# Kernel tuning notes

Measured on AMD Instinct MI355X. Metric: run time of the kernel, lower is better.

Reference implementation:

```python
import jax, jax.numpy as jnp
import numpy as np

N_C = 50000
N_N = 50000
E = 500000
D = 128


def _graph_conv(x_src, src, dst, n_src, n_dst, W, b):
    # DGL GraphConv, norm='both': symmetric degree normalization, then linear.
    ones = jnp.ones(src.shape, x_src.dtype)
    deg_out = jax.ops.segment_sum(ones, src, num_segments=n_src)
    deg_in = jax.ops.segment_sum(ones, dst, num_segments=n_dst)
    norm_src = jnp.maximum(deg_out, 1.0) ** -0.5  # [n_src]
    norm_dst = jnp.maximum(deg_in, 1.0) ** -0.5   # [n_dst]
    m = (x_src * norm_src[:, None])[src]          # [E, D] gather
    agg = jax.ops.segment_sum(m, dst, num_segments=n_dst)  # [n_dst, D]
    return (agg * norm_dst[:, None]) @ W + b


def _sage_conv(x_src, x_dst, src, dst, n_dst, W_self, W_neigh, b):
    # DGL SAGEConv, aggregator='mean': fc_self(h_dst) + fc_neigh(mean_neigh) + bias.
    ones = jnp.ones(src.shape, x_src.dtype)
    deg_in = jnp.maximum(jax.ops.segment_sum(ones, dst, num_segments=n_dst), 1.0)
    h_neigh = jax.ops.segment_sum(x_src[src], dst, num_segments=n_dst) / deg_in[:, None]
    return x_dst @ W_self + h_neigh @ W_neigh + b


def setup_inputs() -> dict:
    key = jax.random.key(0)
    ks = jax.random.split(key, 20)
    s = 1.0 / np.sqrt(D)
    inp = {
        'feat_C': jax.random.normal(ks[0], (N_C, D), jnp.float32),
        'feat_N': jax.random.normal(ks[1], (N_N, D), jnp.float32),
        'W1_cc': jax.random.normal(ks[2], (D, D), jnp.float32) * s,
        'b1_cc': jnp.zeros((D,), jnp.float32),
        'W1_cn': jax.random.normal(ks[3], (D, D), jnp.float32) * s,
        'b1_cn': jnp.zeros((D,), jnp.float32),
        'W1_self': jax.random.normal(ks[4], (D, D), jnp.float32) * s,
        'W1_neigh': jax.random.normal(ks[5], (D, D), jnp.float32) * s,
        'b1_nn': jnp.zeros((D,), jnp.float32),
        'W2_cc': jax.random.normal(ks[6], (D, D), jnp.float32) * s,
        'b2_cc': jnp.zeros((D,), jnp.float32),
        'W2_cn': jax.random.normal(ks[7], (D, D), jnp.float32) * s,
        'b2_cn': jnp.zeros((D,), jnp.float32),
        'W2_self': jax.random.normal(ks[8], (D, D), jnp.float32) * s,
        'W2_neigh': jax.random.normal(ks[9], (D, D), jnp.float32) * s,
        'b2_nn': jnp.zeros((D,), jnp.float32),
        'cc_src': jax.random.randint(ks[10], (E,), 0, N_C),
        'cc_dst': jax.random.randint(ks[11], (E,), 0, N_C),
        'cn_src': jax.random.randint(ks[12], (E,), 0, N_C),
        'cn_dst': jax.random.randint(ks[13], (E,), 0, N_N),
        'nn_src': jax.random.randint(ks[14], (E,), 0, N_N),
        'nn_dst': jax.random.randint(ks[15], (E,), 0, N_N),
    }
    return inp


def reference(feat_C, feat_N, W1_cc, b1_cc, W1_cn, b1_cn, W1_self, W1_neigh, b1_nn,
              W2_cc, b2_cc, W2_cn, b2_cn, W2_self, W2_neigh, b2_nn,
              cc_src, cc_dst, cn_src, cn_dst, nn_src, nn_dst):
    # layer 1 (HeteroGraphConv, aggregate='sum') + relu
    hC = _graph_conv(feat_C, cc_src, cc_dst, N_C, N_C, W1_cc, b1_cc)
    hN = (_graph_conv(feat_C, cn_src, cn_dst, N_C, N_N, W1_cn, b1_cn)
          + _sage_conv(feat_N, feat_N, nn_src, nn_dst, N_N, W1_self, W1_neigh, b1_nn))
    hC = jax.nn.relu(hC)
    hN = jax.nn.relu(hN)
    # layer 2
    oC = _graph_conv(hC, cc_src, cc_dst, N_C, N_C, W2_cc, b2_cc)
    oN = (_graph_conv(hC, cn_src, cn_dst, N_C, N_N, W2_cn, b2_cn)
          + _sage_conv(hN, hN, nn_src, nn_dst, N_N, W2_self, W2_neigh, b2_nn))
    return oC, oN
```

## Files before the change

kernel.cpp:

```cpp
#include <hip/hip_runtime.h>

#define NCN 50000
#define NE  500000
#define DF  128

#define BSHIFT 9
#define NBUCK 98
#define BK 128
#define CAP 7168
#define CHUNK 4096

typedef __attribute__((ext_vector_type(8))) short mfrag;
typedef __attribute__((ext_vector_type(4))) float facc4;

__device__ inline ushort f2bf(float x) {
    unsigned u = __float_as_uint(x);
    unsigned r = (u + 0x7FFFu + ((u >> 16) & 1u)) >> 16;
    return (ushort)r;
}
__device__ inline float bf2f(ushort h) { return __uint_as_float(((unsigned)h) << 16); }

__device__ inline void store_split4m(ushort* __restrict__ T, int row, int lane4,
                                     float4 v, int mode) {
    ushort h0 = f2bf(v.x); ushort l0 = f2bf(v.x - bf2f(h0));
    ushort h1 = f2bf(v.y); ushort l1 = f2bf(v.y - bf2f(h1));
    ushort h2 = f2bf(v.z); ushort l2 = f2bf(v.z - bf2f(h2));
    ushort h3 = f2bf(v.w); ushort l3 = f2bf(v.w - bf2f(h3));
    uint2 hp = make_uint2((uint)h0 | ((uint)h1 << 16), (uint)h2 | ((uint)h3 << 16));
    uint2 lp = make_uint2((uint)l0 | ((uint)l1 << 16), (uint)l2 | ((uint)l3 << 16));
    size_t hiOff, loOff;
    if (mode == 0) { hiOff = (size_t)row * DF; loOff = (size_t)NCN * DF + (size_t)row * DF; }
    else           { hiOff = (size_t)row * 256; loOff = hiOff + 128; }
    *(uint2*)(T + hiOff + lane4 * 4) = hp;
    *(uint2*)(T + loOff + lane4 * 4) = lp;
}

__global__ __launch_bounds__(256) void hist2_k(
    const int* __restrict__ cc_src, const int* __restrict__ cn_src,
    int* __restrict__ cnt2)
{
    int i = blockIdx.x * 256 + threadIdx.x;
    if (i >= NE) return;
    atomicAdd(&cnt2[cc_src[i]], 1);
    atomicAdd(&cnt2[NCN + cn_src[i]], 1);
}

__global__ __launch_bounds__(256) void srcnorm_k(
    const int* __restrict__ cnt2, float* __restrict__ snorm2, int n2)
{
    int i = blockIdx.x * 256 + threadIdx.x;
    if (i >= n2) return;
    int c = cnt2[i]; if (c < 1) c = 1;
    snorm2[i] = rsqrtf((float)c);
}

__global__ __launch_bounds__(256) void binA_k(
    const int* __restrict__ cc_src, const int* __restrict__ cc_dst,
    const int* __restrict__ cn_src, const int* __restrict__ cn_dst,
    const int* __restrict__ nn_src, const int* __restrict__ nn_dst,
    uint2* __restrict__ R, int* __restrict__ bc)
{
    const int s = blockIdx.y;
    const int* key; const int* pay;
    switch (s) {
      case 0: key = cc_dst; pay = cc_src; break;
      case 1: key = cn_dst; pay = cn_src; break;
      default: key = nn_dst; pay = nn_src; break;
    }
    __shared__ uint2 rec[CHUNK];
    __shared__ int lhist[BK], lofs[BK], lcur[BK], gbase[BK];
    __shared__ int ls[256];
    const int tid = threadIdx.x;
    const int base = blockIdx.x * CHUNK;

    int k[16], p[16];
    #pragma unroll
    for (int j = 0; j < 16; ++j) {
        int e = base + j * 256 + tid;
        bool valid = (e < NE);
        k[j] = valid ? key[e] : -1;
        p[j] = valid ? pay[e] : 0;
    }
    if (tid < BK) lhist[tid] = 0;
    __syncthreads();
    #pragma unroll
    for (int j = 0; j < 16; ++j)
        if (k[j] >= 0) atomicAdd(&lhist[k[j] >> BSHIFT], 1);
    __syncthreads();
    int v = (tid < BK) ? lhist[tid] : 0;
    ls[tid] = v;
    __syncthreads();
    #pragma unroll
    for (int off = 1; off < 128; off <<= 1) {
        int t = (tid >= off) ? ls[tid - off] : 0;
        __syncthreads();
        ls[tid] += t;
        __syncthreads();
    }
    if (tid < BK) { int e = ls[tid] - v; lofs[tid] = e; lcur[tid] = e; }
    __syncthreads();
    #pragma unroll
    for (int j = 0; j < 16; ++j) {
        if (k[j] >= 0) {
            int b = k[j] >> BSHIFT;
            int pos = atomicAdd(&lcur[b], 1);
            rec[pos] = make_uint2((unsigned)k[j], (unsigned)p[j]);
        }
    }
    __syncthreads();
    if (tid < BK) {
        int c = lcur[tid] - lofs[tid];
        gbase[tid] = (c > 0) ? atomicAdd(&bc[s * BK + tid], c) : 0;
    }
    __syncthreads();
    int total = ls[127];
    for (int i = tid; i < total; i += 256) {
        uint2 r = rec[i];
        int b = (int)(r.x >> BSHIFT);
        int gi = gbase[b] + (i - lofs[b]);
        R[((size_t)s * NBUCK + b) * CAP + gi] = r;
    }
}

__global__ __launch_bounds__(256) void binB_k(
    const uint2* __restrict__ R, const int* __restrict__ bc,
    int* __restrict__ rp3, int* __restrict__ col3)
{
    const int b = blockIdx.x;
    const int s = blockIdx.y;
    const int tid = threadIdx.x;
    __shared__ int cnt[512];
    __shared__ int lofs[512];
    __shared__ int ls[256];
    __shared__ int sbase;

    const int nrec = bc[s * BK + b];
    const uint2* rec = R + ((size_t)s * NBUCK + b) * CAP;

    for (int i = tid; i < 512; i += 256) cnt[i] = 0;
    __syncthreads();
    for (int i = tid; i < nrec; i += 256)
        atomicAdd(&cnt[rec[i].x & 511], 1);
    __syncthreads();

    {
        int v = (tid < b) ? bc[s * BK + tid] : 0;
        ls[tid] = v;
        __syncthreads();
        for (int off = 128; off > 0; off >>= 1) {
            if (tid < off) ls[tid] += ls[tid + off];
            __syncthreads();
        }
        if (tid == 0) sbase = ls[0];
        __syncthreads();
    }
    const int colBase = sbase;

    int v0 = cnt[2 * tid], v1 = cnt[2 * tid + 1];
    int pairSum = v0 + v1;
    ls[tid] = pairSum;
    __syncthreads();
    #pragma unroll
    for (int off = 1; off < 256; off <<= 1) {
        int t = (tid >= off) ? ls[tid - off] : 0;
        __syncthreads();
        ls[tid] += t;
        __syncthreads();
    }
    int excl = ls[tid] - pairSum;
    lofs[2 * tid] = excl;
    lofs[2 * tid + 1] = excl + v0;
    __syncthreads();
    const int total = ls[255];

    int* rp = rp3 + (size_t)s * (NCN + 1);
    for (int j = tid; j < 512; j += 256) {
        int d = b * 512 + j;
        if (d < NCN) rp[d] = colBase + lofs[j];
    }
    if (b == NBUCK - 1 && tid == 0) rp[NCN] = colBase + total;
    __syncthreads();

    int* col = col3 + (size_t)s * NE + colBase;
    for (int i = tid; i < nrec; i += 256) {
        uint2 r = rec[i];
        int pos = atomicAdd(&lofs[r.x & 511], 1);
        col[pos] = (int)r.y;
    }
}

__global__ __launch_bounds__(256) void wconv_k(
    const float* __restrict__ Wm0, const float* __restrict__ Wm1,
    const float* __restrict__ Wm2, const float* __restrict__ Wm3,
    const float* __restrict__ Wm4, const float* __restrict__ Wm5,
    const float* __restrict__ Wm6, const float* __restrict__ Wm7,
    ushort* __restrict__ out)
{
    const float* Ws[8] = {Wm0, Wm1, Wm2, Wm3, Wm4, Wm5, Wm6, Wm7};
    const float* W = Ws[blockIdx.x];
    ushort* o = out + (size_t)blockIdx.x * 32768;
    for (int i = threadIdx.x; i < 16384; i += 256) {
        int c = i >> 13;
        int r = i & 8191;
        int n = r >> 6;
        int jj = r & 63;
        int kk = c * 64 + (jj ^ ((n & 7) << 3));
        float wv = W[kk * 128 + n];
        ushort h = f2bf(wv);
        float lv = wv - bf2f(h);
        o[c * 16384 + r] = h;
        o[c * 16384 + 8192 + r] = f2bf(lv);
    }
}

__global__ __launch_bounds__(256) void agg_k(
    const float* __restrict__ X0, const int* __restrict__ rp0,
    const int* __restrict__ col0, const float* __restrict__ sc0,
    ushort* __restrict__ out0, int m0,
    const float* __restrict__ X1, const int* __restrict__ rp1,
    const int* __restrict__ col1, const float* __restrict__ sc1,
    ushort* __restrict__ out1, int m1,
    const float* __restrict__ X2, const int* __restrict__ rp2,
    const int* __restrict__ col2, const float* __restrict__ sc2,
    ushort* __restrict__ out2, int m2)
{
    const float* X; const int* rp; const int* col; const float* sc; ushort* out; int mode;
    if (blockIdx.y == 0)      { X = X0; rp = rp0; col = col0; sc = sc0; out = out0; mode = m0; }
    else if (blockIdx.y == 1) { X = X1; rp = rp1; col = col1; sc = sc1; out = out1; mode = m1; }
    else                      { X = X2; rp = rp2; col = col2; sc = sc2; out = out2; mode = m2; }

    int wid = (blockIdx.x * 256 + threadIdx.x) >> 6;
    int half = (threadIdx.x >> 5) & 1;
    int lane4 = threadIdx.x & 31;
    int row = wid * 2 + half;
    if (row >= NCN) return;
    int e0 = rp[row], e1 = rp[row + 1];
    const bool useSc = (sc != nullptr);
    float4 a = make_float4(0.f, 0.f, 0.f, 0.f);
    int e = e0;
    while (e < e1) {
        int cnt = e1 - e; if (cnt > 32) cnt = 32;
        int myc = (lane4 < cnt) ? col[e + lane4] : 0;
        float mysc = (useSc && lane4 < cnt) ? sc[myc] : 1.0f;
        int j = 0;
        for (; j + 4 <= cnt; j += 4) {
            int s0 = __shfl(myc, j, 32),     s1 = __shfl(myc, j + 1, 32);
            int s2 = __shfl(myc, j + 2, 32), s3 = __shfl(myc, j + 3, 32);
            float c0 = __shfl(mysc, j, 32),     c1 = __shfl(mysc, j + 1, 32);
            float c2 = __shfl(mysc, j + 2, 32), c3 = __shfl(mysc, j + 3, 32);
            const float4 u0 = *(const float4*)(X + (size_t)s0 * DF + lane4 * 4);
            const float4 u1 = *(const float4*)(X + (size_t)s1 * DF + lane4 * 4);
            const float4 u2 = *(const float4*)(X + (size_t)s2 * DF + lane4 * 4);
            const float4 u3 = *(const float4*)(X + (size_t)s3 * DF + lane4 * 4);
            a.x = fmaf(u0.x, c0, a.x); a.y = fmaf(u0.y, c0, a.y);
            a.z = fmaf(u0.z, c0, a.z); a.w = fmaf(u0.w, c0, a.w);
            a.x = fmaf(u1.x, c1, a.x); a.y = fmaf(u1.y, c1, a.y);
            a.z = fmaf(u1.z, c1, a.z); a.w = fmaf(u1.w, c1, a.w);
            a.x = fmaf(u2.x, c2, a.x); a.y = fmaf(u2.y, c2, a.y);
            a.z = fmaf(u2.z, c2, a.z); a.w = fmaf(u2.w, c2, a.w);
            a.x = fmaf(u3.x, c3, a.x); a.y = fmaf(u3.y, c3, a.y);
            a.z = fmaf(u3.z, c3, a.z); a.w = fmaf(u3.w, c3, a.w);
        }
        for (; j < cnt; ++j) {
            int s0 = __shfl(myc, j, 32);
            float c0 = __shfl(mysc, j, 32);
            const float4 u0 = *(const float4*)(X + (size_t)s0 * DF + lane4 * 4);
            a.x = fmaf(u0.x, c0, a.x); a.y = fmaf(u0.y, c0, a.y);
            a.z = fmaf(u0.z, c0, a.z); a.w = fmaf(u0.w, c0, a.w);
        }
        e += cnt;
    }
    int deg = e1 - e0; if (deg < 1) deg = 1;
    float dsc = useSc ? rsqrtf((float)deg) : (1.0f / (float)deg);
    a.x *= dsc; a.y *= dsc; a.z *= dsc; a.w *= dsc;
    store_split4m(out, row, lane4, a, mode);
}

template<int NSRC, bool RELU, int F32S, bool A1INT>
__device__ __forceinline__ void gemm_body(
    ushort* __restrict__ Wsm,
    const void* __restrict__ A0, const void* __restrict__ A1, const void* __restrict__ A2,
    const ushort* __restrict__ Wi0, const ushort* __restrict__ Wi1, const ushort* __restrict__ Wi2,
    const float* __restrict__ b0, const float* __restrict__ b1,
    float* __restrict__ Y)
{
    constexpr int NCH = 2 * NSRC;
    const int tid = threadIdx.x;
    const int l = tid & 63;
    const int wv = tid >> 6;
    const int r0 = blockIdx.x * 128;
    const int M = NCN;

    const void*   Aarr[3] = {A0, A1, A2};
    const ushort* Warr[3] = {Wi0, Wi1, Wi2};

    int arow[2];
    #pragma unroll
    for (int rt = 0; rt < 2; ++rt) {
        int r = r0 + wv * 32 + rt * 16 + (l & 15);
        arow[rt] = (r < M) ? r : (M - 1);
    }
    const int kgrp = (l >> 4) * 8;

    facc4 acc[2][8];
    #pragma unroll
    for (int rt = 0; rt < 2; ++rt)
        #pragma unroll
        for (int ct = 0; ct < 8; ++ct)
            acc[rt][ct] = (facc4){0.f, 0.f, 0.f, 0.f};

    uint4 Wr[8];
    auto loadWr = [&](int c) {
        int s = c >> 1, chalf = c & 1;
        const uint4* wp = (const uint4*)(Warr[s] + chalf * 16384);
        #pragma unroll
        for (int i = 0; i < 8; ++i) Wr[i] = wp[i * 256 + tid];
    };

    mfrag ah[2][2], al[2][2];
    auto loadA = [&](int c) {
        int s = c >> 1;
        int k0 = (c & 1) * 64;
        if (s == F32S) {
            const float* F = (const float*)Aarr[s];
            #pragma unroll
            for (int ks = 0; ks < 2; ++ks)
                #pragma unroll
                for (int rt = 0; rt < 2; ++rt) {
                    const float* p = F + (size_t)arow[rt] * DF + k0 + ks * 32 + kgrp;
                    float4 v0 = *(const float4*)p;
                    float4 v1 = *(const float4*)(p + 4);
                    union { mfrag m; ushort u[8]; } H, L;
                    float vv0[4] = {v0.x, v0.y, v0.z, v0.w};
                    float vv1[4] = {v1.x, v1.y, v1.z, v1.w};
                    #pragma unroll
                    for (int j = 0; j < 4; ++j) {
                        ushort h = f2bf(vv0[j]);
                        H.u[j] = h; L.u[j] = f2bf(vv0[j] - bf2f(h));
                    }
                    #pragma unroll
                    for (int j = 0; j < 4; ++j) {
                        ushort h = f2bf(vv1[j]);
                        H.u[4 + j] = h; L.u[4 + j] = f2bf(vv1[j] - bf2f(h));
                    }
                    ah[ks][rt] = H.m; al[ks][rt] = L.m;
                }
        } else {
            const ushort* T = (const ushort*)Aarr[s];
            const bool INT = (s == 1 && A1INT);
            const int rs = INT ? 256 : DF;
            const size_t lo = INT ? 128 : (size_t)NCN * DF;
            #pragma unroll
            for (int ks = 0; ks < 2; ++ks)
                #pragma unroll
                for (int rt = 0; rt < 2; ++rt) {
                    size_t o = (size_t)arow[rt] * rs + k0 + ks * 32 + kgrp;
                    ah[ks][rt] = *(const mfrag*)(T + o);
                    al[ks][rt] = *(const mfrag*)(T + o + lo);
                }
        }
    };

    loadWr(0);
    #pragma unroll
    for (int c = 0; c < NCH; ++c) {
        __syncthreads();
        {
            uint4* wd = (uint4*)Wsm;
            #pragma unroll
            for (int i = 0; i < 8; ++i) wd[i * 256 + tid] = Wr[i];
        }
        loadA(c);
        if (c + 1 < NCH) loadWr(c + 1);
        __syncthreads();
        #pragma unroll
        for (int ks = 0; ks < 2; ++ks) {
            const int kbyte = ks * 64 + (l >> 4) * 16;
            #pragma unroll
            for (int ct = 0; ct < 8; ++ct) {
                int colc = ct * 16 + (l & 15);
                int widx = colc * 64 + ((kbyte ^ ((colc & 7) << 4)) >> 1);
                mfrag w_hi = *(const mfrag*)(Wsm + widx);
                mfrag w_lo = *(const mfrag*)(Wsm + 8192 + widx);
                #pragma unroll
                for (int rt = 0; rt < 2; ++rt) {
                    acc[rt][ct] = __builtin_amdgcn_mfma_f32_16x16x32_bf16(ah[ks][rt], w_hi, acc[rt][ct], 0, 0, 0);
                    acc[rt][ct] = __builtin_amdgcn_mfma_f32_16x16x32_bf16(ah[ks][rt], w_lo, acc[rt][ct], 0, 0, 0);
                    acc[rt][ct] = __builtin_amdgcn_mfma_f32_16x16x32_bf16(al[ks][rt], w_hi, acc[rt][ct], 0, 0, 0);
                }
            }
        }
    }
    __syncthreads();

    float bias[8];
    #pragma unroll
    for (int ct = 0; ct < 8; ++ct) {
        int colc = ct * 16 + (l & 15);
        float bv = b0 ? b0[colc] : 0.f;
        if (b1) bv += b1[colc];
        bias[ct] = bv;
    }
    #pragma unroll
    for (int rt = 0; rt < 2; ++rt) {
        #pragma unroll
        for (int q = 0; q < 4; ++q) {
            int row = r0 + wv * 32 + rt * 16 + (l >> 4) * 4 + q;
            if (row < M) {
                #pragma unroll
                for (int ct = 0; ct < 8; ++ct) {
                    float v = acc[rt][ct][q] + bias[ct];
                    if (RELU) v = fmaxf(v, 0.f);
                    Y[(size_t)row * DF + ct * 16 + (l & 15)] = v;
                }
            }
        }
    }
}

template<bool RELU, bool A1INT>
__global__ __launch_bounds__(256, 3) void fgemm2_k(
    const ushort* __restrict__ AN0, const ushort* __restrict__ AN1,
    const float* __restrict__ AN2f,
    const ushort* __restrict__ WiN0, const ushort* __restrict__ WiN1,
    const ushort* __restrict__ WiN2,
    const float* __restrict__ bN0, const float* __restrict__ bN1,
    float* __restrict__ YN,
    const ushort* __restrict__ AC0, const ushort* __restrict__ WiC,
    const float* __restrict__ bC, float* __restrict__ YC)
{
    __shared__ ushort Wsm[16384];
    if (blockIdx.z == 0)
        gemm_body<3, RELU, 2, A1INT>(Wsm, AN0, AN1, AN2f, WiN0, WiN1, WiN2,
                                     bN0, bN1, YN);
    else
        gemm_body<1, RELU, -1, false>(Wsm, AC0, nullptr, nullptr,
                                      WiC, nullptr, nullptr, bC, nullptr, YC);
}

template<bool RELU>
__global__ __launch_bounds__(256, 3) void gemmN_k(
    const ushort* __restrict__ A0, const ushort* __restrict__ A1i,
    const float* __restrict__ A2f,
    const ushort* __restrict__ Wi0, const ushort* __restrict__ Wi1,
    const ushort* __restrict__ Wi2,
    const float* __restrict__ b0, const float* __restrict__ b1,
    float* __restrict__ Y)
{
    __shared__ ushort Wsm[16384];
    gemm_body<3, RELU, 2, true>(Wsm, A0, A1i, A2f, Wi0, Wi1, Wi2, b0, b1, Y);
}

template<bool RELU>
__global__ __launch_bounds__(256, 3) void gemmC_k(
    const ushort* __restrict__ A0, const ushort* __restrict__ Wi0,
    const float* __restrict__ b0, float* __restrict__ Y)
{
    __shared__ ushort Wsm[16384];
    gemm_body<1, RELU, -1, false>(Wsm, A0, nullptr, nullptr, Wi0, nullptr, nullptr,
                                  b0, nullptr, Y);
}

extern "C" void kernel_launch(void* const* d_in, const int* in_sizes, int n_in,
                              void* d_out, int out_size, void* d_ws, size_t ws_size,
                              hipStream_t stream)
{
    (void)in_sizes; (void)n_in; (void)out_size;
    const float* feat_C   = (const float*)d_in[0];
    const float* feat_N   = (const float*)d_in[1];
    const float* W1_cc    = (const float*)d_in[2];
    const float* b1_cc    = (const float*)d_in[3];
    const float* W1_cn    = (const float*)d_in[4];
    const float* b1_cn    = (const float*)d_in[5];
    const float* W1_self  = (const float*)d_in[6];
    const float* W1_neigh = (const float*)d_in[7];
    const float* b1_nn    = (const float*)d_in[8];
    const float* W2_cc    = (const float*)d_in[9];
    const float* b2_cc    = (const float*)d_in[10];
    const float* W2_cn    = (const float*)d_in[11];
    const float* b2_cn    = (const float*)d_in[12];
    const float* W2_self  = (const float*)d_in[13];
    const float* W2_neigh = (const float*)d_in[14];
    const float* b2_nn    = (const float*)d_in[15];
    const int* cc_src = (const int*)d_in[16];
    const int* cc_dst = (const int*)d_in[17];
    const int* cn_src = (const int*)d_in[18];
    const int* cn_dst = (const int*)d_in[19];
    const int* nn_src = (const int*)d_in[20];
    const int* nn_dst = (const int*)d_in[21];

    char* ws = (char*)d_ws;
    size_t off = 0;
    auto take = [&](size_t bytes) -> char* {
        char* p = ws + off;
        off = (off + bytes + 255) & ~(size_t)255;
        return p;
    };
    const size_t TBL = (size_t)2 * NCN * DF * sizeof(ushort);
    int*    rp3    = (int*)take((size_t)3 * (NCN + 1) * sizeof(int));
    int*    col3   = (int*)take((size_t)3 * NE * sizeof(int));
    float*  snorm2 = (float*)take((size_t)2 * NCN * sizeof(float));
    int*    cnt2   = (int*)take((size_t)2 * NCN * sizeof(int));
    int*    bc     = (int*)take((size_t)3 * BK * sizeof(int));
    ushort* Wimg   = (ushort*)take((size_t)8 * 32768 * sizeof(ushort));
    char* bigRegion = take(2 * TBL);
    uint2*  R  = (uint2*)bigRegion;
    ushort* P0 = (ushort*)bigRegion;
    ushort* P1 = (ushort*)(bigRegion + TBL);
    const bool useP2 = (ws_size >= off + TBL);
    ushort* P2 = useP2 ? (ushort*)take(TBL) : nullptr;

    float* oC = (float*)d_out;
    float* oN = oC + (size_t)NCN * DF;
    ushort* oC_us = (ushort*)oC;
    ushort* oN_us = (ushort*)oN;

    const int edgeBlocks = (NE + 255) / 256;
    const int binABlocks = (NE + CHUNK - 1) / CHUNK;
    const int aggBlocks  = (((NCN + 1) / 2) * 64 + 255) / 256;
    const int gemmBlocks = (NCN + 127) / 128;

    auto img = [&](int m) { return (const ushort*)(Wimg + (size_t)m * 32768); };
    const int* rpCC = rp3 + 0 * (NCN + 1);
    const int* rpCN = rp3 + 1 * (NCN + 1);
    const int* rpNN = rp3 + 2 * (NCN + 1);
    const int* colCC = col3 + 0 * NE;
    const int* colCN = col3 + 1 * NE;
    const int* colNN = col3 + 2 * NE;
    const float* snCC = snorm2 + 0 * NCN;
    const float* snCN = snorm2 + 1 * NCN;

    hipMemsetAsync(cnt2, 0, (size_t)2 * NCN * sizeof(int), stream);
    hipMemsetAsync(bc, 0, (size_t)3 * BK * sizeof(int), stream);
    hist2_k<<<edgeBlocks, 256, 0, stream>>>(cc_src, cn_src, cnt2);
    srcnorm_k<<<(2 * NCN + 255) / 256, 256, 0, stream>>>(cnt2, snorm2, 2 * NCN);
    binA_k<<<dim3(binABlocks, 3), 256, 0, stream>>>(cc_src, cc_dst, cn_src, cn_dst,
                                                    nn_src, nn_dst, R, bc);
    binB_k<<<dim3(NBUCK, 3), 256, 0, stream>>>(R, bc, rp3, col3);
    wconv_k<<<8, 256, 0, stream>>>(W1_cc, W1_cn, W1_neigh, W1_self,
                                   W2_cc, W2_cn, W2_neigh, W2_self, Wimg);

    if (useP2) {
        agg_k<<<dim3(aggBlocks, 3), 256, 0, stream>>>(
            feat_C, rpCC, colCC, snCC, P0, 0,
            feat_C, rpCN, colCN, snCN, P1, 0,
            feat_N, rpNN, colNN, nullptr, P2, 0);
        fgemm2_k<true, false><<<dim3(gemmBlocks, 1, 2), 256, 0, stream>>>(
            P1, P2, feat_N, img(1), img(2), img(3), b1_cn, b1_nn, oN,
            P0, img(0), b1_cc, oC);
        agg_k<<<dim3(aggBlocks, 3), 256, 0, stream>>>(
            oC, rpCC, colCC, snCC, P0, 0,
            oC, rpCN, colCN, snCN, P1, 0,
            oN, rpNN, colNN, nullptr, P2, 0);
        fgemm2_k<false, false><<<dim3(gemmBlocks, 1, 2), 256, 0, stream>>>(
            P1, P2, oN, img(5), img(6), img(7), b2_cn, b2_nn, oN,
            P0, img(4), b2_cc, oC);
    } else {
        agg_k<<<dim3(aggBlocks, 3), 256, 0, stream>>>(
            feat_C, rpCC, colCC, snCC, P0, 0,
            feat_C, rpCN, colCN, snCN, P1, 0,
            feat_N, rpNN, colNN, nullptr, oN_us, 1);
        fgemm2_k<true, true><<<dim3(gemmBlocks, 1, 2), 256, 0, stream>>>(
            P1, oN_us, feat_N, img(1), img(2), img(3), b1_cn, b1_nn, oN,
            P0, img(0), b1_cc, oC);
        agg_k<<<dim3(aggBlocks, 2), 256, 0, stream>>>(
            oC, rpCC, colCC, snCC, P0, 0,
            oC, rpCN, colCN, snCN, P1, 0,
            nullptr, nullptr, nullptr, nullptr, nullptr, 0);
        agg_k<<<dim3(aggBlocks, 1), 256, 0, stream>>>(
            oN, rpNN, colNN, nullptr, oC_us, 1,
            nullptr, nullptr, nullptr, nullptr, nullptr, 0,
            nullptr, nullptr, nullptr, nullptr, nullptr, 0);
        gemmN_k<false><<<gemmBlocks, 256, 0, stream>>>(P1, oC_us, oN,
                                                       img(5), img(6), img(7),
                                                       b2_cn, b2_nn, oN);
        gemmC_k<false><<<gemmBlocks, 256, 0, stream>>>(P0, img(4), b2_cc, oC);
    }
}
```

Measured before the change: 432.4 us.

## Read split-bf16 weights directly from global memory instead of staging through LDS

The GEMM kernels drop the shared-memory weight staging, with its double-buffered register prefetch and two barriers per K-chunk. Each wave now loads its MFMA B fragments straight from global memory, relying on L1/L2 caching of the small weight matrices. The weight-conversion kernel drops the XOR swizzle to match the plain layout, and launch bounds go from 3 to 4 blocks per CU. This removes LDS traffic and synchronisation but makes every wave re-fetch weights from cache, and the extra global loads could stall the MFMAs.

```diff
diff --git a/kernel.cpp b/kernel.cpp
--- a/kernel.cpp
+++ b/kernel.cpp
@@ -204,7 +204,7 @@
         int r = i & 8191;
         int n = r >> 6;
         int jj = r & 63;
-        int kk = c * 64 + (jj ^ ((n & 7) << 3));
+        int kk = c * 64 + jj;
         float wv = W[kk * 128 + n];
         ushort h = f2bf(wv);
         float lv = wv - bf2f(h);
@@ -278,7 +278,6 @@
 
 template<int NSRC, bool RELU, int F32S, bool A1INT>
 __device__ __forceinline__ void gemm_body(
-    ushort* __restrict__ Wsm,
     const void* __restrict__ A0, const void* __restrict__ A1, const void* __restrict__ A2,
     const ushort* __restrict__ Wi0, const ushort* __restrict__ Wi1, const ushort* __restrict__ Wi2,
     const float* __restrict__ b0, const float* __restrict__ b1,
@@ -301,6 +300,7 @@
         arow[rt] = (r < M) ? r : (M - 1);
     }
     const int kgrp = (l >> 4) * 8;
+    const int wlane = (l & 15) * 64 + kgrp;
 
     facc4 acc[2][8];
     #pragma unroll
@@ -309,22 +309,16 @@
         for (int ct = 0; ct < 8; ++ct)
             acc[rt][ct] = (facc4){0.f, 0.f, 0.f, 0.f};
 
-    uint4 Wr[8];
-    auto loadWr = [&](int c) {
-        int s = c >> 1, chalf = c & 1;
-        const uint4* wp = (const uint4*)(Warr[s] + chalf * 16384);
+    #pragma unroll
+    for (int c = 0; c < NCH; ++c) {
+        const int s = c >> 1;
+        const int k0 = (c & 1) * 64;
+        const ushort* Wc = Warr[s] + (c & 1) * 16384;
         #pragma unroll
-        for (int i = 0; i < 8; ++i) Wr[i] = wp[i * 256 + tid];
-    };
-
-    mfrag ah[2][2], al[2][2];
-    auto loadA = [&](int c) {
-        int s = c >> 1;
-        int k0 = (c & 1) * 64;
-        if (s == F32S) {
-            const float* F = (const float*)Aarr[s];
-            #pragma unroll
-            for (int ks = 0; ks < 2; ++ks)
+        for (int ks = 0; ks < 2; ++ks) {
+            mfrag ah[2], al[2];
+            if (s == F32S) {
+                const float* F = (const float*)Aarr[s];
                 #pragma unroll
                 for (int rt = 0; rt < 2; ++rt) {
                     const float* p = F + (size_t)arow[rt] * DF + k0 + ks * 32 + kgrp;
@@ -343,50 +337,30 @@
                         ushort h = f2bf(vv1[j]);
                         H.u[4 + j] = h; L.u[4 + j] = f2bf(vv1[j] - bf2f(h));
                     }
-                    ah[ks][rt] = H.m; al[ks][rt] = L.m;
+                    ah[rt] = H.m; al[rt] = L.m;
                 }
-        } else {
-            const ushort* T = (const ushort*)Aarr[s];
-            const bool INT = (s == 1 && A1INT);
-            const int rs = INT ? 256 : DF;
-            const size_t lo = INT ? 128 : (size_t)NCN * DF;
-            #pragma unroll
-            for (int ks = 0; ks < 2; ++ks)
+            } else {
+                const ushort* T = (const ushort*)Aarr[s];
+                const bool INT = (s == 1 && A1INT);
+                const int rs = INT ? 256 : DF;
+                const size_t lo = INT ? 128 : (size_t)NCN * DF;
                 #pragma unroll
                 for (int rt = 0; rt < 2; ++rt) {
                     size_t o = (size_t)arow[rt] * rs + k0 + ks * 32 + kgrp;
-                    ah[ks][rt] = *(const mfrag*)(T + o);
-                    al[ks][rt] = *(const mfrag*)(T + o + lo);
+                    ah[rt] = *(const mfrag*)(T + o);
+                    al[rt] = *(const mfrag*)(T + o + lo);
                 }
-        }
-    };
-
-    loadWr(0);
-    #pragma unroll
-    for (int c = 0; c < NCH; ++c) {
-        __syncthreads();
-        {
-            uint4* wd = (uint4*)Wsm;
-            #pragma unroll
-            for (int i = 0; i < 8; ++i) wd[i * 256 + tid] = Wr[i];
-        }
-        loadA(c);
-        if (c + 1 < NCH) loadWr(c + 1);
-        __syncthreads();
-        #pragma unroll
-        for (int ks = 0; ks < 2; ++ks) {
-            const int kbyte = ks * 64 + (l >> 4) * 16;
+            }
+            const ushort* wbase = Wc + ks * 32 + wlane;
             #pragma unroll
             for (int ct = 0; ct < 8; ++ct) {
-                int colc = ct * 16 + (l & 15);
-                int widx = colc * 64 + ((kbyte ^ ((colc & 7) << 4)) >> 1);
-                mfrag w_hi = *(const mfrag*)(Wsm + widx);
-                mfrag w_lo = *(const mfrag*)(Wsm + 8192 + widx);
+                mfrag w_hi = *(const mfrag*)(wbase + ct * 1024);
+                mfrag w_lo = *(const mfrag*)(wbase + ct * 1024 + 8192);
                 #pragma unroll
                 for (int rt = 0; rt < 2; ++rt) {
-                    acc[rt][ct] = __builtin_amdgcn_mfma_f32_16x16x32_bf16(ah[ks][rt], w_hi, acc[rt][ct], 0, 0, 0);
-                    acc[rt][ct] = __builtin_amdgcn_mfma_f32_16x16x32_bf16(ah[ks][rt], w_lo, acc[rt][ct], 0, 0, 0);
-                    acc[rt][ct] = __builtin_amdgcn_mfma_f32_16x16x32_bf16(al[ks][rt], w_hi, acc[rt][ct], 0, 0, 0);
+                    acc[rt][ct] = __builtin_amdgcn_mfma_f32_16x16x32_bf16(ah[rt], w_hi, acc[rt][ct], 0, 0, 0);
+                    acc[rt][ct] = __builtin_amdgcn_mfma_f32_16x16x32_bf16(ah[rt], w_lo, acc[rt][ct], 0, 0, 0);
+                    acc[rt][ct] = __builtin_amdgcn_mfma_f32_16x16x32_bf16(al[rt], w_hi, acc[rt][ct], 0, 0, 0);
                 }
             }
         }
@@ -419,7 +393,7 @@
 }
 
 template<bool RELU, bool A1INT>
-__global__ __launch_bounds__(256, 3) void fgemm2_k(
+__global__ __launch_bounds__(256, 4) void fgemm2_k(
     const ushort* __restrict__ AN0, const ushort* __restrict__ AN1,
     const float* __restrict__ AN2f,
     const ushort* __restrict__ WiN0, const ushort* __restrict__ WiN1,
@@ -429,17 +403,16 @@
     const ushort* __restrict__ AC0, const ushort* __restrict__ WiC,
     const float* __restrict__ bC, float* __restrict__ YC)
 {
-    __shared__ ushort Wsm[16384];
     if (blockIdx.z == 0)
-        gemm_body<3, RELU, 2, A1INT>(Wsm, AN0, AN1, AN2f, WiN0, WiN1, WiN2,
+        gemm_body<3, RELU, 2, A1INT>(AN0, AN1, AN2f, WiN0, WiN1, WiN2,
                                      bN0, bN1, YN);
     else
-        gemm_body<1, RELU, -1, false>(Wsm, AC0, nullptr, nullptr,
+        gemm_body<1, RELU, -1, false>(AC0, nullptr, nullptr,
                                       WiC, nullptr, nullptr, bC, nullptr, YC);
 }
 
 template<bool RELU>
-__global__ __launch_bounds__(256, 3) void gemmN_k(
+__global__ __launch_bounds__(256, 4) void gemmN_k(
     const ushort* __restrict__ A0, const ushort* __restrict__ A1i,
     const float* __restrict__ A2f,
     const ushort* __restrict__ Wi0, const ushort* __restrict__ Wi1,
@@ -447,17 +420,15 @@
     const float* __restrict__ b0, const float* __restrict__ b1,
     float* __restrict__ Y)
 {
-    __shared__ ushort Wsm[16384];
-    gemm_body<3, RELU, 2, true>(Wsm, A0, A1i, A2f, Wi0, Wi1, Wi2, b0, b1, Y);
+    gemm_body<3, RELU, 2, true>(A0, A1i, A2f, Wi0, Wi1, Wi2, b0, b1, Y);
 }
 
 template<bool RELU>
-__global__ __launch_bounds__(256, 3) void gemmC_k(
+__global__ __launch_bounds__(256, 4) void gemmC_k(
     const ushort* __restrict__ A0, const ushort* __restrict__ Wi0,
     const float* __restrict__ b0, float* __restrict__ Y)
 {
-    __shared__ ushort Wsm[16384];
-    gemm_body<1, RELU, -1, false>(Wsm, A0, nullptr, nullptr, Wi0, nullptr, nullptr,
+    gemm_body<1, RELU, -1, false>(A0, nullptr, nullptr, Wi0, nullptr, nullptr,
                                   b0, nullptr, Y);
 }
 
```

Result: slower. 478.1 us (+10.6%).

## Retile GEMM warps to 64x64 subtiles and double-buffer A fragments

Applied to the files above, without the earlier changes.

Each wave now computes a 64-row by 64-column subtile (4x4 MFMA tiles) instead of 32 rows by all 128 columns. This halves the shared-memory weight fragment reads per MFMA and cuts redundant weight traffic per wave. A loads are split per k-step into two register buffers so the second half's global loads overlap the first half's compute. Register pressure rises, so launch bounds drop from 3 to 2 blocks per CU, which lowers occupancy.

```diff
diff --git a/kernel.cpp b/kernel.cpp
--- a/kernel.cpp
+++ b/kernel.cpp
@@ -288,25 +288,27 @@
     const int tid = threadIdx.x;
     const int l = tid & 63;
     const int wv = tid >> 6;
+    const int wvr = wv & 1;
+    const int wvc = wv >> 1;
     const int r0 = blockIdx.x * 128;
     const int M = NCN;
 
     const void*   Aarr[3] = {A0, A1, A2};
     const ushort* Warr[3] = {Wi0, Wi1, Wi2};
 
-    int arow[2];
-    #pragma unroll
-    for (int rt = 0; rt < 2; ++rt) {
-        int r = r0 + wv * 32 + rt * 16 + (l & 15);
+    int arow[4];
+    #pragma unroll
+    for (int rt = 0; rt < 4; ++rt) {
+        int r = r0 + wvr * 64 + rt * 16 + (l & 15);
         arow[rt] = (r < M) ? r : (M - 1);
     }
     const int kgrp = (l >> 4) * 8;
 
-    facc4 acc[2][8];
-    #pragma unroll
-    for (int rt = 0; rt < 2; ++rt)
+    facc4 acc[4][4];
+    #pragma unroll
+    for (int rt = 0; rt < 4; ++rt)
         #pragma unroll
-        for (int ct = 0; ct < 8; ++ct)
+        for (int ct = 0; ct < 4; ++ct)
             acc[rt][ct] = (facc4){0.f, 0.f, 0.f, 0.f};
 
     uint4 Wr[8];
@@ -317,47 +319,60 @@
         for (int i = 0; i < 8; ++i) Wr[i] = wp[i * 256 + tid];
     };
 
-    mfrag ah[2][2], al[2][2];
-    auto loadA = [&](int c) {
+    mfrag ahA[4], alA[4], ahB[4], alB[4];
+    auto loadA = [&](int c, int ks, mfrag (&ah)[4], mfrag (&al)[4]) {
         int s = c >> 1;
-        int k0 = (c & 1) * 64;
+        int k0 = (c & 1) * 64 + ks * 32;
         if (s == F32S) {
             const float* F = (const float*)Aarr[s];
             #pragma unroll
-            for (int ks = 0; ks < 2; ++ks)
+            for (int rt = 0; rt < 4; ++rt) {
+                const float* p = F + (size_t)arow[rt] * DF + k0 + kgrp;
+                float4 v0 = *(const float4*)p;
+                float4 v1 = *(const float4*)(p + 4);
+                union { mfrag m; ushort u[8]; } H, L;
+                float vv0[4] = {v0.x, v0.y, v0.z, v0.w};
+                float vv1[4] = {v1.x, v1.y, v1.z, v1.w};
                 #pragma unroll
-                for (int rt = 0; rt < 2; ++rt) {
-                    const float* p = F + (size_t)arow[rt] * DF + k0 + ks * 32 + kgrp;
-                    float4 v0 = *(const float4*)p;
-                    float4 v1 = *(const float4*)(p + 4);
-                    union { mfrag m; ushort u[8]; } H, L;
-                    float vv0[4] = {v0.x, v0.y, v0.z, v0.w};
-                    float vv1[4] = {v1.x, v1.y, v1.z, v1.w};
-                    #pragma unroll
-                    for (int j = 0; j < 4; ++j) {
-                        ushort h = f2bf(vv0[j]);
-                        H.u[j] = h; L.u[j] = f2bf(vv0[j] - bf2f(h));
-                    }
-                    #pragma unroll
-                    for (int j = 0; j < 4; ++j) {
-                        ushort h = f2bf(vv1[j]);
-                        H.u[4 + j] = h; L.u[4 + j] = f2bf(vv1[j] - bf2f(h));
-                    }
-                    ah[ks][rt] = H.m; al[ks][rt] = L.m;
+                for (int j = 0; j < 4; ++j) {
+                    ushort h = f2bf(vv0[j]);
+                    H.u[j] = h; L.u[j] = f2bf(vv0[j] - bf2f(h));
                 }
+                #pragma unroll
+                for (int j = 0; j < 4; ++j) {
+                    ushort h = f2bf(vv1[j]);
+                    H.u[4 + j] = h; L.u[4 + j] = f2bf(vv1[j] - bf2f(h));
+                }
+                ah[rt] = H.m; al[rt] = L.m;
+            }
         } else {
             const ushort* T = (const ushort*)Aarr[s];
             const bool INT = (s == 1 && A1INT);
             const int rs = INT ? 256 : DF;
             const size_t lo = INT ? 128 : (size_t)NCN * DF;
             #pragma unroll
-            for (int ks = 0; ks < 2; ++ks)
-                #pragma unroll
-                for (int rt = 0; rt < 2; ++rt) {
-                    size_t o = (size_t)arow[rt] * rs + k0 + ks * 32 + kgrp;
-                    ah[ks][rt] = *(const mfrag*)(T + o);
-                    al[ks][rt] = *(const mfrag*)(T + o + lo);
-                }
+            for (int rt = 0; rt < 4; ++rt) {
+                size_t o = (size_t)arow[rt] * rs + k0 + kgrp;
+                ah[rt] = *(const mfrag*)(T + o);
+                al[rt] = *(const mfrag*)(T + o + lo);
+            }
+        }
+    };
+
+    auto compute = [&](int ks, const mfrag (&ah)[4], const mfrag (&al)[4]) {
+        const int kbyte = ks * 64 + (l >> 4) * 16;
+        #pragma unroll
+        for (int ct = 0; ct < 4; ++ct) {
+            int colc = wvc * 64 + ct * 16 + (l & 15);
+            int widx = colc * 64 + ((kbyte ^ ((colc & 7) << 4)) >> 1);
+            mfrag w_hi = *(const mfrag*)(Wsm + widx);
+            mfrag w_lo = *(const mfrag*)(Wsm + 8192 + widx);
+            #pragma unroll
+            for (int rt = 0; rt < 4; ++rt) {
+                acc[rt][ct] = __builtin_amdgcn_mfma_f32_16x16x32_bf16(ah[rt], w_hi, acc[rt][ct], 0, 0, 0);
+                acc[rt][ct] = __builtin_amdgcn_mfma_f32_16x16x32_bf16(ah[rt], w_lo, acc[rt][ct], 0, 0, 0);
+                acc[rt][ct] = __builtin_amdgcn_mfma_f32_16x16x32_bf16(al[rt], w_hi, acc[rt][ct], 0, 0, 0);
+            }
         }
     };
 
@@ -370,48 +385,34 @@
             #pragma unroll
             for (int i = 0; i < 8; ++i) wd[i * 256 + tid] = Wr[i];
         }
-        loadA(c);
+        loadA(c, 0, ahA, alA);
         if (c + 1 < NCH) loadWr(c + 1);
         __syncthreads();
-        #pragma unroll
-        for (int ks = 0; ks < 2; ++ks) {
-            const int kbyte = ks * 64 + (l >> 4) * 16;
-            #pragma unroll
-            for (int ct = 0; ct < 8; ++ct) {
-                int colc = ct * 16 + (l & 15);
-                int widx = colc * 64 + ((kbyte ^ ((colc & 7) << 4)) >> 1);
-                mfrag w_hi = *(const mfrag*)(Wsm + widx);
-                mfrag w_lo = *(const mfrag*)(Wsm + 8192 + widx);
-                #pragma unroll
-                for (int rt = 0; rt < 2; ++rt) {
-                    acc[rt][ct] = __builtin_amdgcn_mfma_f32_16x16x32_bf16(ah[ks][rt], w_hi, acc[rt][ct], 0, 0, 0);
-                    acc[rt][ct] = __builtin_amdgcn_mfma_f32_16x16x32_bf16(ah[ks][rt], w_lo, acc[rt][ct], 0, 0, 0);
-                    acc[rt][ct] = __builtin_amdgcn_mfma_f32_16x16x32_bf16(al[ks][rt], w_hi, acc[rt][ct], 0, 0, 0);
-                }
-            }
-        }
-    }
-    __syncthreads();
-
-    float bias[8];
-    #pragma unroll
-    for (int ct = 0; ct < 8; ++ct) {
-        int colc = ct * 16 + (l & 15);
+        loadA(c, 1, ahB, alB);
+        compute(0, ahA, alA);
+        compute(1, ahB, alB);
+    }
+    __syncthreads();
+
+    float bias[4];
+    #pragma unroll
+    for (int ct = 0; ct < 4; ++ct) {
+        int colc = wvc * 64 + ct * 16 + (l & 15);
         float bv = b0 ? b0[colc] : 0.f;
         if (b1) bv += b1[colc];
         bias[ct] = bv;
     }
     #pragma unroll
-    for (int rt = 0; rt < 2; ++rt) {
+    for (int rt = 0; rt < 4; ++rt) {
         #pragma unroll
         for (int q = 0; q < 4; ++q) {
-            int row = r0 + wv * 32 + rt * 16 + (l >> 4) * 4 + q;
+            int row = r0 + wvr * 64 + rt * 16 + (l >> 4) * 4 + q;
             if (row < M) {
                 #pragma unroll
-                for (int ct = 0; ct < 8; ++ct) {
+                for (int ct = 0; ct < 4; ++ct) {
                     float v = acc[rt][ct][q] + bias[ct];
                     if (RELU) v = fmaxf(v, 0.f);
-                    Y[(size_t)row * DF + ct * 16 + (l & 15)] = v;
+                    Y[(size_t)row * DF + wvc * 64 + ct * 16 + (l & 15)] = v;
                 }
             }
         }
@@ -419,7 +420,7 @@
 }
 
 template<bool RELU, bool A1INT>
-__global__ __launch_bounds__(256, 3) void fgemm2_k(
+__global__ __launch_bounds__(256, 2) void fgemm2_k(
     const ushort* __restrict__ AN0, const ushort* __restrict__ AN1,
     const float* __restrict__ AN2f,
     const ushort* __restrict__ WiN0, const ushort* __restrict__ WiN1,
@@ -439,7 +440,7 @@
 }
 
 template<bool RELU>
-__global__ __launch_bounds__(256, 3) void gemmN_k(
+__global__ __launch_bounds__(256, 2) void gemmN_k(
     const ushort* __restrict__ A0, const ushort* __restrict__ A1i,
     const float* __restrict__ A2f,
     const ushort* __restrict__ Wi0, const ushort* __restrict__ Wi1,
@@ -452,7 +453,7 @@
 }
 
 template<bool RELU>
-__global__ __launch_bounds__(256, 3) void gemmC_k(
+__global__ __launch_bounds__(256, 2) void gemmC_k(
     const ushort* __restrict__ A0, const ushort* __restrict__ Wi0,
     const float* __restrict__ b0, float* __restrict__ Y)
 {
```

After: 435.9 us. About the same (+0.8%).
